# Kernel tuning notes

Hardware: AMD Instinct MI355X
Metric: run time of the kernel (lower is better)

Reference implementation:

```python
import jax, jax.numpy as jnp
import numpy as np

N = 50000          # num nodes
E = 800000         # num edges (avg degree 16)
R = 8              # num relations
IN = 128
H0 = 256
H1 = 64


def _w(key, shape, fan_in):
    return jax.random.normal(key, shape, dtype=jnp.float32) * (1.0 / np.sqrt(fan_in))


def setup_inputs() -> dict:
    key = jax.random.key(0)
    ks = jax.random.split(key, 16)
    x = jax.random.normal(ks[0], (N, IN), dtype=jnp.float32)
    edge_index = jax.random.randint(ks[1], (2, E), 0, N, dtype=jnp.int64)
    edge_type = jax.random.randint(ks[2], (E,), 0, R, dtype=jnp.int64)
    return {
        "x": x,
        "edge_index": edge_index,
        "edge_type": edge_type,
        # RGCNConv params: per-relation weights [R, in, out], root weight [in, out], bias [out]
        "W1": _w(ks[3], (R, IN, H0), IN), "root1": _w(ks[4], (IN, H0), IN), "b1": jnp.zeros((H0,), jnp.float32),
        "W2": _w(ks[5], (R, H0, H0), H0), "root2": _w(ks[6], (H0, H0), H0), "b2": jnp.zeros((H0,), jnp.float32),
        "W3": _w(ks[7], (R, H0, H0), H0), "root3": _w(ks[8], (H0, H0), H0), "b3": jnp.zeros((H0,), jnp.float32),
        "W4": _w(ks[9], (R, H0, H1), H0), "root4": _w(ks[10], (H0, H1), H0), "b4": jnp.zeros((H1,), jnp.float32),
    }


def rgcn_layer(x, edge_index, edge_type, W, root, bias):
    """PyG RGCNConv: out_i = x_i @ root + sum_r (1/|N_r(i)|) sum_{j in N_r(i)} x_j @ W_r + bias.
    Aggregation is linear, so aggregate source features per (relation, dst) first,
    then apply the R small GEMMs — avoids per-edge [E, out] message materialization."""
    src, dst = edge_index[0], edge_index[1]
    seg = edge_type * N + dst                      # combined (relation, dst) segment id
    nseg = R * N
    agg = jax.ops.segment_sum(x[src], seg, num_segments=nseg)          # [R*N, in]
    cnt = jax.ops.segment_sum(jnp.ones((seg.shape[0],), x.dtype), seg, num_segments=nseg)
    agg = agg / jnp.maximum(cnt, 1.0)[:, None]                          # mean per (r, i)
    agg = agg.reshape(R, N, x.shape[1])                                 # [R, N, in]
    return jnp.einsum('rni,rio->no', agg, W) + x @ root + bias


def reference(x, edge_index, edge_type, W1, root1, b1, W2, root2, b2, W3, root3, b3, W4, root4, b4):
    h = jax.nn.relu(rgcn_layer(x, edge_index, edge_type, W1, root1, b1))
    h = jax.nn.relu(rgcn_layer(h, edge_index, edge_type, W2, root2, b2))
    h = jax.nn.relu(rgcn_layer(h, edge_index, edge_type, W3, root3, b3))
    return rgcn_layer(h, edge_index, edge_type, W4, root4, b4)
```

## Files before the change

kernel.cpp:

```cpp
#include <hip/hip_runtime.h>

#define N_NODES 50000
#define N_PAD   50048
#define N_EDGES 800000
#define N_REL   8
#define NSEG    (N_REL * N_NODES)
#define SCAN_NB 391

typedef short bf16x8 __attribute__((ext_vector_type(8)));
typedef float f32x4  __attribute__((ext_vector_type(4)));

__device__ __forceinline__ ushort f2bf(float f) {
    union { float f; unsigned u; } c; c.f = f;
    unsigned u = c.u + 0x7fffu + ((c.u >> 16) & 1u);
    return (ushort)(u >> 16);
}
__device__ __forceinline__ void add8(float* s, uint4 v) {
    unsigned u[4] = {v.x, v.y, v.z, v.w};
    #pragma unroll
    for (int k = 0; k < 4; ++k) {
        s[2 * k]     += __uint_as_float(u[k] << 16);
        s[2 * k + 1] += __uint_as_float(u[k] & 0xffff0000u);
    }
}
__device__ __forceinline__ void async16(const ushort* g, ushort* l) {
    __builtin_amdgcn_global_load_lds((const __attribute__((address_space(1))) void*)g,
                                     (__attribute__((address_space(3))) void*)l, 16, 0, 0);
}


__global__ void count_edges(const int* __restrict__ dst, const int* __restrict__ et,
                            int* __restrict__ cnt) {
    int e = blockIdx.x * 256 + threadIdx.x;
    if (e < N_EDGES) atomicAdd(&cnt[et[e] * N_NODES + dst[e]], 1);
}

__global__ __launch_bounds__(256) void scan_pass1(const int* __restrict__ cnt,
                                                  int* __restrict__ sums) {
    __shared__ int sc[256];
    int b = blockIdx.x, t = threadIdx.x;
    int base = b * 1024 + t * 4;
    int v = 0;
    #pragma unroll
    for (int i = 0; i < 4; ++i) { int idx = base + i; if (idx < NSEG) v += cnt[idx]; }
    sc[t] = v; __syncthreads();
    for (int off = 1; off < 256; off <<= 1) {
        int x = (t >= off) ? sc[t - off] : 0;
        __syncthreads(); sc[t] += x; __syncthreads();
    }
    if (t == 255) sums[b] = sc[255];
}

__global__ __launch_bounds__(512) void scan_pass2(int* __restrict__ sums, int nb) {
    __shared__ int sc[512];
    int t = threadIdx.x;
    int v = (t < nb) ? sums[t] : 0;
    sc[t] = v; __syncthreads();
    for (int off = 1; off < 512; off <<= 1) {
        int x = (t >= off) ? sc[t - off] : 0;
        __syncthreads(); sc[t] += x; __syncthreads();
    }
    if (t < nb) sums[t] = sc[t] - v;
}

__global__ __launch_bounds__(256) void scan_pass3(const int* __restrict__ cnt,
                                                  const int* __restrict__ sums,
                                                  int* __restrict__ row_ptr) {
    __shared__ int sc[256];
    int b = blockIdx.x, t = threadIdx.x;
    int base = b * 1024 + t * 4;
    int e[4]; int v = 0;
    #pragma unroll
    for (int i = 0; i < 4; ++i) { int idx = base + i; e[i] = (idx < NSEG) ? cnt[idx] : 0; v += e[i]; }
    sc[t] = v; __syncthreads();
    for (int off = 1; off < 256; off <<= 1) {
        int x = (t >= off) ? sc[t - off] : 0;
        __syncthreads(); sc[t] += x; __syncthreads();
    }
    int run = sums[b] + (sc[t] - v);
    #pragma unroll
    for (int i = 0; i < 4; ++i) {
        int idx = base + i;
        if (idx < NSEG) row_ptr[idx] = run;
        run += e[i];
    }
    if (b == 0 && t == 0) row_ptr[NSEG] = N_EDGES;
}

__global__ void place_edges(const int* __restrict__ src, const int* __restrict__ dst,
                            const int* __restrict__ et, const int* __restrict__ row_ptr,
                            int* __restrict__ cnt, int* __restrict__ sorted_src) {
    int e = blockIdx.x * 256 + threadIdx.x;
    if (e >= N_EDGES) return;
    int key = et[e] * N_NODES + dst[e];
    int old = atomicSub(&cnt[key], 1);
    sorted_src[row_ptr[key] + old - 1] = src[e];
}


__global__ void convert_weights(const float* __restrict__ W, const float* __restrict__ root,
                                ushort* __restrict__ BT, int I, int O, int NPAD) {
    int idx = blockIdx.x * 256 + threadIdx.x;
    if (idx >= NPAD * I) return;
    int col = idx / I, i = idx % I;
    float v = 0.0f;
    if (col < N_REL * O) {
        int r = col / O, o = col % O;
        v = W[((size_t)r * I + i) * O + o];
    } else if (col < (N_REL + 1) * O) {
        v = root[(size_t)i * O + (col - N_REL * O)];
    }
    BT[idx] = f2bf(v);
}

__global__ void f32_to_bf16(const float* __restrict__ in, ushort* __restrict__ out, int n4) {
    int i = blockIdx.x * 256 + threadIdx.x;
    if (i >= n4) return;
    float4 v = ((const float4*)in)[i];
    ushort4 s; s.x = f2bf(v.x); s.y = f2bf(v.y); s.z = f2bf(v.z); s.w = f2bf(v.w);
    ((ushort4*)out)[i] = s;
}

template<int K>
__global__ __launch_bounds__(256)
void gemm_mfma(const ushort* __restrict__ A, const ushort* __restrict__ BT,
               ushort* __restrict__ Y, int NW) {
    __shared__ ushort As[128 * 32];
    __shared__ ushort Bs[128 * 32];
    const int t = threadIdx.x;
    const int lane = t & 63;
    const int w = t >> 6;
    const int l16 = lane & 15, q = lane >> 4;
    const int wm = (w & 1) * 64, wn = (w >> 1) * 64;
    const int row0 = blockIdx.x * 128;
    const int col0 = blockIdx.y * 128;

    const int c0i = w * 64 + lane;
    const int c1i = c0i + 256;
    const size_t ga0 = (size_t)(c0i >> 2) * K + (size_t)(c0i & 3) * 8;
    const size_t ga1 = (size_t)(c1i >> 2) * K + (size_t)(c1i & 3) * 8;
    const ushort* Ab = A + (size_t)row0 * K;
    const ushort* Bb = BT + (size_t)col0 * K;
    ushort* lA0 = &As[w * 512];
    ushort* lA1 = &As[(w + 4) * 512];
    ushort* lB0 = &Bs[w * 512];
    ushort* lB1 = &Bs[(w + 4) * 512];

    f32x4 acc[4][4] = {};

    #pragma unroll
    for (int k0 = 0; k0 < K; k0 += 32) {
        __syncthreads();
        async16(Ab + k0 + ga0, lA0);
        async16(Ab + k0 + ga1, lA1);
        async16(Bb + k0 + ga0, lB0);
        async16(Bb + k0 + ga1, lB1);
        __syncthreads();
        bf16x8 a[4], b[4];
        #pragma unroll
        for (int i = 0; i < 4; ++i) {
            a[i] = *(const bf16x8*)&As[(wm + i * 16 + l16) * 32 + q * 8];
            b[i] = *(const bf16x8*)&Bs[(wn + i * 16 + l16) * 32 + q * 8];
        }
        #pragma unroll
        for (int i = 0; i < 4; ++i)
            #pragma unroll
            for (int j = 0; j < 4; ++j)
                acc[i][j] = __builtin_amdgcn_mfma_f32_16x16x32_bf16(a[i], b[j], acc[i][j], 0, 0, 0);
    }

    #pragma unroll
    for (int i = 0; i < 4; ++i) {
        int grow = row0 + wm + i * 16 + q * 4;
        #pragma unroll
        for (int j = 0; j < 4; ++j) {
            int gcol = col0 + wn + j * 16 + l16;
            ushort* p = Y + (size_t)grow * NW + gcol;
            #pragma unroll
            for (int r = 0; r < 4; ++r)
                p[(size_t)r * NW] = f2bf(acc[i][j][r]);
        }
    }
}

template<int O>
__global__ __launch_bounds__(256)
void gather_kernel(const ushort* __restrict__ Y, int NW, int rel0, int nrel, int rootcol,
                   const int* __restrict__ row_ptr, const int* __restrict__ sorted_src,
                   const float* __restrict__ bias, const float* __restrict__ accum,
                   float* __restrict__ out_f32, ushort* __restrict__ out_bf16, int relu) {
    constexpr int TPN = O / 8;
    int d = blockIdx.x * (256 / TPN) + threadIdx.x / TPN;
    if (d >= N_NODES) return;
    int c0 = (threadIdx.x % TPN) * 8;
    float sum[8] = {};
    if (rootcol >= 0) {
        add8(sum, *(const uint4*)(Y + (size_t)d * NW + rootcol + c0));
        #pragma unroll
        for (int k = 0; k < 8; ++k) sum[k] += bias[c0 + k];
    }
    if (accum) {
        const float* ap = accum + (size_t)d * O + c0;
        float4 x0 = *(const float4*)ap, x1 = *(const float4*)(ap + 4);
        sum[0] += x0.x; sum[1] += x0.y; sum[2] += x0.z; sum[3] += x0.w;
        sum[4] += x1.x; sum[5] += x1.y; sum[6] += x1.z; sum[7] += x1.w;
    }
    for (int rr = 0; rr < nrel; ++rr) {
        int base = (rel0 + rr) * N_NODES + d;
        int s0 = row_ptr[base], s1 = row_ptr[base + 1];
        if (s1 <= s0) continue;
        float ps[8] = {};
        const ushort* Yc = Y + rr * O + c0;
        for (int e = s0; e < s1; ++e)
            add8(ps, *(const uint4*)(Yc + (size_t)sorted_src[e] * NW));
        float inv = 1.0f / (float)(s1 - s0);
        #pragma unroll
        for (int k = 0; k < 8; ++k) sum[k] += ps[k] * inv;
    }
    if (relu) {
        #pragma unroll
        for (int k = 0; k < 8; ++k) sum[k] = fmaxf(sum[k], 0.0f);
    }
    if (out_bf16) {
        ushort o[8];
        #pragma unroll
        for (int k = 0; k < 8; ++k) o[k] = f2bf(sum[k]);
        *(uint4*)(out_bf16 + (size_t)d * O + c0) = *(const uint4*)o;
    }
    if (out_f32) {
        float* p = out_f32 + (size_t)d * O + c0;
        *(float4*)p = make_float4(sum[0], sum[1], sum[2], sum[3]);
        *(float4*)(p + 4) = make_float4(sum[4], sum[5], sum[6], sum[7]);
    }
}


static void launch_gemm(int K, const ushort* A, const ushort* BT, ushort* Y, int NW,
                        hipStream_t st) {
    dim3 g(N_PAD / 128, NW / 128), b(256);
    if (K == 128) gemm_mfma<128><<<g, b, 0, st>>>(A, BT, Y, NW);
    else          gemm_mfma<256><<<g, b, 0, st>>>(A, BT, Y, NW);
}

static void launch_gather(int O, const ushort* Y, int NW, int rel0, int nrel, int rootcol,
                          const int* rp, const int* ss, const float* bias, const float* accum,
                          float* of, ushort* ob, int relu, hipStream_t st) {
    if (O == 256)
        gather_kernel<256><<<dim3((N_NODES + 7) / 8), 256, 0, st>>>(Y, NW, rel0, nrel, rootcol,
                                                                    rp, ss, bias, accum, of, ob, relu);
    else
        gather_kernel<64><<<dim3((N_NODES + 31) / 32), 256, 0, st>>>(Y, NW, rel0, nrel, rootcol,
                                                                     rp, ss, bias, accum, of, ob, relu);
}

extern "C" void kernel_launch(void* const* d_in, const int* in_sizes, int n_in,
                              void* d_out, int out_size, void* d_ws, size_t ws_size,
                              hipStream_t stream) {
    const float* x  = (const float*)d_in[0];
    const int*   ei = (const int*)d_in[1];
    const int*   et = (const int*)d_in[2];
    const float* W[4]    = {(const float*)d_in[3], (const float*)d_in[6], (const float*)d_in[9],  (const float*)d_in[12]};
    const float* RT[4]   = {(const float*)d_in[4], (const float*)d_in[7], (const float*)d_in[10], (const float*)d_in[13]};
    const float* BI[4]   = {(const float*)d_in[5], (const float*)d_in[8], (const float*)d_in[11], (const float*)d_in[14]};
    const int KS[4] = {128, 256, 256, 256};
    const int OS[4] = {256, 256, 256, 64};
    const int NP[4] = {2304, 2304, 2304, 640};
    const int* src = ei;
    const int* dst = ei + N_EDGES;

    char* ws = (char*)d_ws;
    size_t off = 0;
    auto take = [&](size_t bytes) -> char* {
        char* p = ws + off;
        off = (off + bytes + 255) & ~(size_t)255;
        return p;
    };
    int* cnt        = (int*)take((size_t)NSEG * 4);
    int* row_ptr    = (int*)take((size_t)(NSEG + 1) * 4);
    int* sums       = (int*)take(512 * 4);
    int* sorted_src = (int*)take((size_t)N_EDGES * 4);
    ushort* BT[4];
    for (int l = 0; l < 4; ++l) BT[l] = (ushort*)take((size_t)NP[l] * KS[l] * 2);
    ushort* hb = (ushort*)take((size_t)N_PAD * 256 * 2);

    const size_t planA_need = off + (size_t)N_PAD * 2304 * 2 + (1u << 20);
    const bool planA = ws_size >= planA_need;
    ushort* Yb; float* hf = nullptr;
    if (planA) {
        Yb = (ushort*)take((size_t)N_PAD * 2304 * 2);
    } else {
        hf = (float*)take((size_t)N_PAD * 256 * 4);
        Yb = (ushort*)take((size_t)N_PAD * 512 * 2);
    }

    hipMemsetAsync(cnt, 0, (size_t)NSEG * 4, stream);
    count_edges<<<(N_EDGES + 255) / 256, 256, 0, stream>>>(dst, et, cnt);
    scan_pass1<<<SCAN_NB, 256, 0, stream>>>(cnt, sums);
    scan_pass2<<<1, 512, 0, stream>>>(sums, SCAN_NB);
    scan_pass3<<<SCAN_NB, 256, 0, stream>>>(cnt, sums, row_ptr);
    place_edges<<<(N_EDGES + 255) / 256, 256, 0, stream>>>(src, dst, et, row_ptr, cnt, sorted_src);

    for (int l = 0; l < 4; ++l) {
        int n = NP[l] * KS[l];
        convert_weights<<<(n + 255) / 256, 256, 0, stream>>>(W[l], RT[l], BT[l], KS[l], OS[l], NP[l]);
    }

    f32_to_bf16<<<(N_NODES * 128 / 4 + 255) / 256, 256, 0, stream>>>(x, hb, N_NODES * 128 / 4);

    for (int l = 0; l < 4; ++l) {
        const int K = KS[l], O = OS[l];
        const bool last = (l == 3);
        float*  of = last ? (float*)d_out : nullptr;
        ushort* ob = last ? nullptr : hb;
        int relu = last ? 0 : 1;
        if (planA) {
            launch_gemm(K, hb, BT[l], Yb, NP[l], stream);
            launch_gather(O, Yb, NP[l], 0, N_REL, N_REL * O, row_ptr, sorted_src,
                          BI[l], nullptr, of, ob, relu, stream);
        } else {
            for (int b = 0; b < 4; ++b) {
                int wdt = 2 * O;
                launch_gemm(K, hb, BT[l] + (size_t)(b * 2 * O) * K, Yb, wdt, stream);
                launch_gather(O, Yb, wdt, b * 2, 2, -1, row_ptr, sorted_src,
                              nullptr, b ? hf : nullptr, hf, nullptr, 0, stream);
            }
            int wr = (O == 256) ? 256 : 128;
            launch_gemm(K, hb, BT[l] + (size_t)(N_REL * O) * K, Yb, wr, stream);
            launch_gather(O, Yb, wr, 0, 0, 0, row_ptr, sorted_src,
                          BI[l], hf, of, ob, relu, stream);
        }
    }
}
```

Measured before the change: 824.0 us.

## Aggregate inputs per relation before GEMM and fuse bias/relu into GEMM epilogue

Switches the order from transform-then-gather to gather-then-transform. Each layer first computes per-relation mean-aggregated input features plus a root copy into a concatenated [N, 9K] bf16 buffer, then runs one GEMM with K=9K against stacked weights. Bias and relu are applied in the GEMM epilogue, which removes the separate gather kernel that read the wide Y buffer. The aim is less gather traffic when the input width is smaller than the output width, and no materialized [N, 9*O] intermediate. The cost is an extra bf16 rounding of the aggregates and a longer GEMM reduction loop that is no longer unrolled.

```diff
diff --git a/kernel.cpp b/kernel.cpp
--- a/kernel.cpp
+++ b/kernel.cpp
@@ -99,16 +99,15 @@
 
 
 __global__ void convert_weights(const float* __restrict__ W, const float* __restrict__ root,
-                                ushort* __restrict__ BT, int I, int O, int NPAD) {
+                                ushort* __restrict__ BT, int K, int O, int NBT) {
+    int KT = 9 * K;
     int idx = blockIdx.x * 256 + threadIdx.x;
-    if (idx >= NPAD * I) return;
-    int col = idx / I, i = idx % I;
+    if (idx >= NBT * KT) return;
+    int col = idx / KT, kk = idx % KT;
     float v = 0.0f;
-    if (col < N_REL * O) {
-        int r = col / O, o = col % O;
-        v = W[((size_t)r * I + i) * O + o];
-    } else if (col < (N_REL + 1) * O) {
-        v = root[(size_t)i * O + (col - N_REL * O)];
+    if (col < O) {
+        int r = kk / K, i = kk % K;
+        v = (r < N_REL) ? W[((size_t)r * K + i) * O + col] : root[(size_t)i * O + col];
     }
     BT[idx] = f2bf(v);
 }
@@ -123,8 +122,36 @@
 
 template<int K>
 __global__ __launch_bounds__(256)
+void segsum_kernel(const ushort* __restrict__ h, const int* __restrict__ row_ptr,
+                   const int* __restrict__ sorted_src, ushort* __restrict__ Agg) {
+    constexpr int TPN = K / 8;
+    constexpr int DPB = 256 / TPN;
+    const int KT = 9 * K;
+    int d = blockIdx.x * DPB + (int)threadIdx.x / TPN;
+    int r = blockIdx.y;
+    int c0 = ((int)threadIdx.x % TPN) * 8;
+    if (d >= N_NODES) return;
+    ushort* outp = Agg + (size_t)d * KT + r * K + c0;
+    if (r == N_REL) {
+        *(uint4*)outp = *(const uint4*)(h + (size_t)d * K + c0);
+        return;
+    }
+    int base = r * N_NODES + d;
+    int s0 = row_ptr[base], s1 = row_ptr[base + 1];
+    float sum[8] = {};
+    for (int e = s0; e < s1; ++e)
+        add8(sum, *(const uint4*)(h + (size_t)sorted_src[e] * K + c0));
+    float inv = (s1 > s0) ? 1.0f / (float)(s1 - s0) : 0.0f;
+    ushort o[8];
+    #pragma unroll
+    for (int k = 0; k < 8; ++k) o[k] = f2bf(sum[k] * inv);
+    *(uint4*)outp = *(const uint4*)o;
+}
+
+__global__ __launch_bounds__(256)
 void gemm_mfma(const ushort* __restrict__ A, const ushort* __restrict__ BT,
-               ushort* __restrict__ Y, int NW) {
+               const float* __restrict__ bias, int KT, int O, int relu,
+               ushort* __restrict__ Cb, float* __restrict__ Cf) {
     __shared__ ushort As[128 * 32];
     __shared__ ushort Bs[128 * 32];
     const int t = threadIdx.x;
@@ -132,15 +159,14 @@
     const int w = t >> 6;
     const int l16 = lane & 15, q = lane >> 4;
     const int wm = (w & 1) * 64, wn = (w >> 1) * 64;
-    const int row0 = blockIdx.x * 128;
-    const int col0 = blockIdx.y * 128;
-
-    const int c0i = w * 64 + lane;
-    const int c1i = c0i + 256;
-    const size_t ga0 = (size_t)(c0i >> 2) * K + (size_t)(c0i & 3) * 8;
-    const size_t ga1 = (size_t)(c1i >> 2) * K + (size_t)(c1i & 3) * 8;
-    const ushort* Ab = A + (size_t)row0 * K;
-    const ushort* Bb = BT + (size_t)col0 * K;
+    const int col0 = blockIdx.x * 128;
+    const int row0 = blockIdx.y * 128;
+
+    const int ci = w * 64 + lane;
+    const size_t ga0 = (size_t)(ci >> 2) * KT + (size_t)((ci & 3) << 3);
+    const ushort* Ab = A + (size_t)row0 * KT;
+    const ushort* Bb = BT + (size_t)col0 * KT;
+    const size_t half = (size_t)64 * KT;
     ushort* lA0 = &As[w * 512];
     ushort* lA1 = &As[(w + 4) * 512];
     ushort* lB0 = &Bs[w * 512];
@@ -148,13 +174,12 @@
 
     f32x4 acc[4][4] = {};
 
-    #pragma unroll
-    for (int k0 = 0; k0 < K; k0 += 32) {
+    for (int k0 = 0; k0 < KT; k0 += 32) {
         __syncthreads();
-        async16(Ab + k0 + ga0, lA0);
-        async16(Ab + k0 + ga1, lA1);
-        async16(Bb + k0 + ga0, lB0);
-        async16(Bb + k0 + ga1, lB1);
+        async16(Ab + ga0 + k0, lA0);
+        async16(Ab + ga0 + half + k0, lA1);
+        async16(Bb + ga0 + k0, lB0);
+        async16(Bb + ga0 + half + k0, lB1);
         __syncthreads();
         bf16x8 a[4], b[4];
         #pragma unroll
@@ -175,83 +200,20 @@
         #pragma unroll
         for (int j = 0; j < 4; ++j) {
             int gcol = col0 + wn + j * 16 + l16;
-            ushort* p = Y + (size_t)grow * NW + gcol;
+            if (gcol >= O) continue;
+            float bv = bias[gcol];
             #pragma unroll
-            for (int r = 0; r < 4; ++r)
-                p[(size_t)r * NW] = f2bf(acc[i][j][r]);
+            for (int r = 0; r < 4; ++r) {
+                float v = acc[i][j][r] + bv;
+                if (relu) v = fmaxf(v, 0.0f);
+                int row = grow + r;
+                if (Cb) Cb[(size_t)row * O + gcol] = f2bf(v);
+                else if (row < N_NODES) Cf[(size_t)row * O + gcol] = v;
+            }
         }
     }
 }
 
-template<int O>
-__global__ __launch_bounds__(256)
-void gather_kernel(const ushort* __restrict__ Y, int NW, int rel0, int nrel, int rootcol,
-                   const int* __restrict__ row_ptr, const int* __restrict__ sorted_src,
-                   const float* __restrict__ bias, const float* __restrict__ accum,
-                   float* __restrict__ out_f32, ushort* __restrict__ out_bf16, int relu) {
-    constexpr int TPN = O / 8;
-    int d = blockIdx.x * (256 / TPN) + threadIdx.x / TPN;
-    if (d >= N_NODES) return;
-    int c0 = (threadIdx.x % TPN) * 8;
-    float sum[8] = {};
-    if (rootcol >= 0) {
-        add8(sum, *(const uint4*)(Y + (size_t)d * NW + rootcol + c0));
-        #pragma unroll
-        for (int k = 0; k < 8; ++k) sum[k] += bias[c0 + k];
-    }
-    if (accum) {
-        const float* ap = accum + (size_t)d * O + c0;
-        float4 x0 = *(const float4*)ap, x1 = *(const float4*)(ap + 4);
-        sum[0] += x0.x; sum[1] += x0.y; sum[2] += x0.z; sum[3] += x0.w;
-        sum[4] += x1.x; sum[5] += x1.y; sum[6] += x1.z; sum[7] += x1.w;
-    }
-    for (int rr = 0; rr < nrel; ++rr) {
-        int base = (rel0 + rr) * N_NODES + d;
-        int s0 = row_ptr[base], s1 = row_ptr[base + 1];
-        if (s1 <= s0) continue;
-        float ps[8] = {};
-        const ushort* Yc = Y + rr * O + c0;
-        for (int e = s0; e < s1; ++e)
-            add8(ps, *(const uint4*)(Yc + (size_t)sorted_src[e] * NW));
-        float inv = 1.0f / (float)(s1 - s0);
-        #pragma unroll
-        for (int k = 0; k < 8; ++k) sum[k] += ps[k] * inv;
-    }
-    if (relu) {
-        #pragma unroll
-        for (int k = 0; k < 8; ++k) sum[k] = fmaxf(sum[k], 0.0f);
-    }
-    if (out_bf16) {
-        ushort o[8];
-        #pragma unroll
-        for (int k = 0; k < 8; ++k) o[k] = f2bf(sum[k]);
-        *(uint4*)(out_bf16 + (size_t)d * O + c0) = *(const uint4*)o;
-    }
-    if (out_f32) {
-        float* p = out_f32 + (size_t)d * O + c0;
-        *(float4*)p = make_float4(sum[0], sum[1], sum[2], sum[3]);
-        *(float4*)(p + 4) = make_float4(sum[4], sum[5], sum[6], sum[7]);
-    }
-}
-
-
-static void launch_gemm(int K, const ushort* A, const ushort* BT, ushort* Y, int NW,
-                        hipStream_t st) {
-    dim3 g(N_PAD / 128, NW / 128), b(256);
-    if (K == 128) gemm_mfma<128><<<g, b, 0, st>>>(A, BT, Y, NW);
-    else          gemm_mfma<256><<<g, b, 0, st>>>(A, BT, Y, NW);
-}
-
-static void launch_gather(int O, const ushort* Y, int NW, int rel0, int nrel, int rootcol,
-                          const int* rp, const int* ss, const float* bias, const float* accum,
-                          float* of, ushort* ob, int relu, hipStream_t st) {
-    if (O == 256)
-        gather_kernel<256><<<dim3((N_NODES + 7) / 8), 256, 0, st>>>(Y, NW, rel0, nrel, rootcol,
-                                                                    rp, ss, bias, accum, of, ob, relu);
-    else
-        gather_kernel<64><<<dim3((N_NODES + 31) / 32), 256, 0, st>>>(Y, NW, rel0, nrel, rootcol,
-                                                                     rp, ss, bias, accum, of, ob, relu);
-}
 
 extern "C" void kernel_launch(void* const* d_in, const int* in_sizes, int n_in,
                               void* d_out, int out_size, void* d_ws, size_t ws_size,
@@ -259,12 +221,12 @@
     const float* x  = (const float*)d_in[0];
     const int*   ei = (const int*)d_in[1];
     const int*   et = (const int*)d_in[2];
-    const float* W[4]    = {(const float*)d_in[3], (const float*)d_in[6], (const float*)d_in[9],  (const float*)d_in[12]};
-    const float* RT[4]   = {(const float*)d_in[4], (const float*)d_in[7], (const float*)d_in[10], (const float*)d_in[13]};
-    const float* BI[4]   = {(const float*)d_in[5], (const float*)d_in[8], (const float*)d_in[11], (const float*)d_in[14]};
-    const int KS[4] = {128, 256, 256, 256};
-    const int OS[4] = {256, 256, 256, 64};
-    const int NP[4] = {2304, 2304, 2304, 640};
+    const float* W[4]  = {(const float*)d_in[3], (const float*)d_in[6], (const float*)d_in[9],  (const float*)d_in[12]};
+    const float* RT[4] = {(const float*)d_in[4], (const float*)d_in[7], (const float*)d_in[10], (const float*)d_in[13]};
+    const float* BI[4] = {(const float*)d_in[5], (const float*)d_in[8], (const float*)d_in[11], (const float*)d_in[14]};
+    const int KS[4]  = {128, 256, 256, 256};
+    const int OS[4]  = {256, 256, 256, 64};
+    const int NBT[4] = {256, 256, 256, 128};
     const int* src = ei;
     const int* dst = ei + N_EDGES;
 
@@ -279,19 +241,10 @@
     int* row_ptr    = (int*)take((size_t)(NSEG + 1) * 4);
     int* sums       = (int*)take(512 * 4);
     int* sorted_src = (int*)take((size_t)N_EDGES * 4);
-    ushort* BT[4];
-    for (int l = 0; l < 4; ++l) BT[l] = (ushort*)take((size_t)NP[l] * KS[l] * 2);
-    ushort* hb = (ushort*)take((size_t)N_PAD * 256 * 2);
-
-    const size_t planA_need = off + (size_t)N_PAD * 2304 * 2 + (1u << 20);
-    const bool planA = ws_size >= planA_need;
-    ushort* Yb; float* hf = nullptr;
-    if (planA) {
-        Yb = (ushort*)take((size_t)N_PAD * 2304 * 2);
-    } else {
-        hf = (float*)take((size_t)N_PAD * 256 * 4);
-        Yb = (ushort*)take((size_t)N_PAD * 512 * 2);
-    }
+    ushort* BTp[4];
+    for (int l = 0; l < 4; ++l) BTp[l] = (ushort*)take((size_t)NBT[l] * 9 * KS[l] * 2);
+    ushort* hb  = (ushort*)take((size_t)N_PAD * 256 * 2);
+    ushort* Agg = (ushort*)take((size_t)N_PAD * 2304 * 2);
 
     hipMemsetAsync(cnt, 0, (size_t)NSEG * 4, stream);
     count_edges<<<(N_EDGES + 255) / 256, 256, 0, stream>>>(dst, et, cnt);
@@ -301,33 +254,21 @@
     place_edges<<<(N_EDGES + 255) / 256, 256, 0, stream>>>(src, dst, et, row_ptr, cnt, sorted_src);
 
     for (int l = 0; l < 4; ++l) {
-        int n = NP[l] * KS[l];
-        convert_weights<<<(n + 255) / 256, 256, 0, stream>>>(W[l], RT[l], BT[l], KS[l], OS[l], NP[l]);
+        int n = NBT[l] * 9 * KS[l];
+        convert_weights<<<(n + 255) / 256, 256, 0, stream>>>(W[l], RT[l], BTp[l], KS[l], OS[l], NBT[l]);
     }
 
     f32_to_bf16<<<(N_NODES * 128 / 4 + 255) / 256, 256, 0, stream>>>(x, hb, N_NODES * 128 / 4);
 
     for (int l = 0; l < 4; ++l) {
-        const int K = KS[l], O = OS[l];
+        const int K = KS[l], O = OS[l], KT = 9 * K;
         const bool last = (l == 3);
-        float*  of = last ? (float*)d_out : nullptr;
-        ushort* ob = last ? nullptr : hb;
-        int relu = last ? 0 : 1;
-        if (planA) {
-            launch_gemm(K, hb, BT[l], Yb, NP[l], stream);
-            launch_gather(O, Yb, NP[l], 0, N_REL, N_REL * O, row_ptr, sorted_src,
-                          BI[l], nullptr, of, ob, relu, stream);
-        } else {
-            for (int b = 0; b < 4; ++b) {
-                int wdt = 2 * O;
-                launch_gemm(K, hb, BT[l] + (size_t)(b * 2 * O) * K, Yb, wdt, stream);
-                launch_gather(O, Yb, wdt, b * 2, 2, -1, row_ptr, sorted_src,
-                              nullptr, b ? hf : nullptr, hf, nullptr, 0, stream);
-            }
-            int wr = (O == 256) ? 256 : 128;
-            launch_gemm(K, hb, BT[l] + (size_t)(N_REL * O) * K, Yb, wr, stream);
-            launch_gather(O, Yb, wr, 0, 0, 0, row_ptr, sorted_src,
-                          BI[l], hf, of, ob, relu, stream);
-        }
-    }
-}
+        if (K == 128)
+            segsum_kernel<128><<<dim3((N_NODES + 15) / 16, 9), 256, 0, stream>>>(hb, row_ptr, sorted_src, Agg);
+        else
+            segsum_kernel<256><<<dim3((N_NODES + 7) / 8, 9), 256, 0, stream>>>(hb, row_ptr, sorted_src, Agg);
+        gemm_mfma<<<dim3(NBT[l] / 128, N_PAD / 128), 256, 0, stream>>>(
+            Agg, BTp[l], BI[l], KT, O, last ? 0 : 1,
+            last ? nullptr : hb, last ? (float*)d_out : nullptr);
+    }
+}
```

Result: slower. 950.7 us (+15.4%).
